# Performance work log

Measured on AMD Instinct MI355X. Metric: run time of the kernel, lower is better.

Reference implementation:

```python
import jax, jax.numpy as jnp
import numpy as np
from jax import lax

KS = 5           # gaussian kernel size
PAD = KS // 2
WINDOW_SIZES = (1, 3, 5)
LN_EPS = 1e-5


def _layernorm(x, g, b):
    m = jnp.mean(x, axis=-1, keepdims=True)
    v = jnp.var(x, axis=-1, keepdims=True)
    return (x - m) * lax.rsqrt(v + LN_EPS) * g + b


def _find_best_interval(p):
    # p: (bs, L). Replicates the sequential strictly-greater update over
    # window sizes [1,3,5] and starts 0..L-w: first candidate (in that order)
    bs, L = p.shape
    amax = jnp.argmax(p, axis=1)                                   # (bs,)
    cs = jnp.concatenate([jnp.zeros((bs, 1), p.dtype), jnp.cumsum(p, axis=1)], axis=1)
    scores, starts, widths = [], [], []
    for w in WINDOW_SIZES:
        if w > L // 2:
            continue
        st = jnp.arange(L - w + 1)
        s = cs[:, st + w] - cs[:, st]                              # sliding sums
        contains = (amax[:, None] >= st[None, :]) & (amax[:, None] < st[None, :] + w)
        scores.append(jnp.where(contains, s, -jnp.inf))
        starts.append(st)
        widths.append(jnp.full((L - w + 1,), w, dtype=jnp.int32))
    S = jnp.concatenate(scores, axis=1)                            # (bs, n_cand)
    starts = jnp.concatenate(starts)
    widths = jnp.concatenate(widths)
    best = jnp.argmax(S, axis=1)
    s0 = starts[best]
    e0 = s0 + widths[best]
    return jnp.stack([s0, e0], axis=1)                             # (bs, 2)


def _forward(v, qa, vp_g, vp_b, vp_W, vp_bias, qp_g, qp_b, qp_W, qp_bias,
             gr_g, gr_b, gr_W1, gr_b1, gr_W2, gr_b2, sigma):
    # v: (bs, L, D), qa: (bs, D). Linears stored as (in, out).
    v2 = jax.nn.gelu(_layernorm(v, vp_g, vp_b) @ vp_W + vp_bias, approximate=False)
    qa2 = jax.nn.gelu(_layernorm(qa, qp_g, qp_b) @ qp_W + qp_bias, approximate=False)
    gate = jnp.tanh(jnp.einsum('bld,bd->bl', v2, qa2))[..., None]  # (bs, L, 1)
    h = _layernorm(v2 * gate, gr_g, gr_b)
    h = jax.nn.gelu(h @ gr_W1 + gr_b1, approximate=False)
    logits = h @ gr_W2 + gr_b2                                     # (bs, L, 1)
    kp = jax.nn.softmax(logits, axis=1)                            # softmax over frames
    # adaptive gaussian smoothing over frames
    x = jnp.arange(KS, dtype=jnp.float32) - KS // 2
    kern = jnp.exp(-0.5 * (x / sigma) ** 2)
    kern = (kern / kern.sum()).reshape(1, 1, KS)
    sm = lax.conv_general_dilated(kp.transpose(0, 2, 1), kern, (1,), [(PAD, PAD)],
                                  dimension_numbers=('NCH', 'OIH', 'NCH')).transpose(0, 2, 1)
    gs = jax.nn.softmax(sm, axis=1)[..., 0]                        # (bs, L)
    max_idx = _find_best_interval(gs)
    bs, L = gs.shape
    rng = jnp.arange(L)[None, :]
    mask = (rng >= max_idx[:, 0:1]) & (rng <= max_idx[:, 1:2])
    start_t = max_idx[:, 0].astype(jnp.float32) / 31.0
    end_t = max_idx[:, 1].astype(jnp.float32) / 31.0
    ori_key = logits[..., 0]
    return gs, max_idx, start_t, end_t, mask, ori_key


def setup_inputs() -> dict:
    key = jax.random.key(0)
    ks = jax.random.split(key, 8)
    BS, L, D = 4096, 32, 768
    H = D // 2
    s = 0.02
    return {
        'v': jax.random.normal(ks[0], (BS, L, D), jnp.float32),
        'qa': jax.random.normal(ks[1], (BS, D), jnp.float32),
        'vp_g': jnp.ones((D,), jnp.float32), 'vp_b': jnp.zeros((D,), jnp.float32),
        'vp_W': jax.random.normal(ks[2], (D, D), jnp.float32) * s,
        'vp_bias': jnp.zeros((D,), jnp.float32),
        'qp_g': jnp.ones((D,), jnp.float32), 'qp_b': jnp.zeros((D,), jnp.float32),
        'qp_W': jax.random.normal(ks[3], (D, D), jnp.float32) * s,
        'qp_bias': jnp.zeros((D,), jnp.float32),
        'gr_g': jnp.ones((D,), jnp.float32), 'gr_b': jnp.zeros((D,), jnp.float32),
        'gr_W1': jax.random.normal(ks[4], (D, H), jnp.float32) * s,
        'gr_b1': jnp.zeros((H,), jnp.float32),
        'gr_W2': jax.random.normal(ks[5], (H, 1), jnp.float32) * s,
        'gr_b2': jnp.zeros((1,), jnp.float32),
        'sigma': jnp.asarray(1.0, jnp.float32),
    }


def reference(v, qa, vp_g, vp_b, vp_W, vp_bias, qp_g, qp_b, qp_W, qp_bias,
              gr_g, gr_b, gr_W1, gr_b1, gr_W2, gr_b2, sigma):
    return _forward(v, qa, vp_g, vp_b, vp_W, vp_bias, qp_g, qp_b, qp_W, qp_bias,
                    gr_g, gr_b, gr_W1, gr_b1, gr_W2, gr_b2, sigma)
```

## Files before the change

kernel.cpp:

```cpp
#include <hip/hip_runtime.h>
#include <math.h>

#define DD 768
#define HH 384
#define LL 32
#define BSZ 4096
#define CAP 256
#define EPS_DEC 4e-7

typedef _Float16 half8 __attribute__((ext_vector_type(8)));
typedef _Float16 half4 __attribute__((ext_vector_type(4)));
typedef float floatx4 __attribute__((ext_vector_type(4)));

static __device__ __forceinline__ float geluf(float x) {
    return 0.5f * x * (1.0f + erff(x * 0.70710678118654752440f));
}
static __device__ __forceinline__ double gelud(double x) {
    return 0.5 * x * (1.0 + erf(x * 0.70710678118654752440));
}

static __device__ void tail_fp64(const double* lgd, double sigma, double* gsd,
                                 int* pst, int* pen, int* pflag, double eps) {
    double kern[5];
    {
        double inv = 1.0 / sigma, ssum = 0.;
#pragma unroll
        for (int j = 0; j < 5; j++) {
            double t = (double)(j - 2) * inv;
            kern[j] = exp(-0.5 * t * t);
            ssum += kern[j];
        }
#pragma unroll
        for (int j = 0; j < 5; j++) kern[j] /= ssum;
    }
    double kp[32];
    {
        double mx = lgd[0];
        for (int i = 1; i < 32; i++) mx = fmax(mx, lgd[i]);
        double sum = 0.;
        for (int i = 0; i < 32; i++) { kp[i] = exp(lgd[i] - mx); sum += kp[i]; }
        for (int i = 0; i < 32; i++) kp[i] /= sum;
    }
    double sm[32];
    for (int i = 0; i < 32; i++) {
        double a = 0.;
#pragma unroll
        for (int j = 0; j < 5; j++) {
            int t = i + j - 2;
            if (t >= 0 && t < 32) a += kern[j] * kp[t];
        }
        sm[i] = a;
    }
    {
        double mx = sm[0];
        for (int i = 1; i < 32; i++) mx = fmax(mx, sm[i]);
        double sum = 0.;
        for (int i = 0; i < 32; i++) { gsd[i] = exp(sm[i] - mx); sum += gsd[i]; }
        for (int i = 0; i < 32; i++) gsd[i] /= sum;
    }
    int am = 0;
    double bv = gsd[0];
    for (int i = 1; i < 32; i++)
        if (gsd[i] > bv) { bv = gsd[i]; am = i; }
    int flag = 0;
    if (eps > 0.) {
        double second = -INFINITY;
        for (int i = 0; i < 32; i++)
            if (i != am && gsd[i] > second) second = gsd[i];
        if (bv - second < eps) flag = 1;
    }
    double cs[33];
    cs[0] = 0.;
    double c = 0.;
    for (int i = 0; i < 32; i++) { c += gsd[i]; cs[i + 1] = c; }
    double best = -INFINITY;
    int bs0 = 0, be0 = 0;
    const int wsz[3] = {1, 3, 5};
    for (int wi = 0; wi < 3; wi++) {
        int w = wsz[wi];
        for (int st = 0; st <= 32 - w; st++) {
            if (am >= st && am < st + w) {
                double sc = cs[st + w] - cs[st];
                if (sc > best) { best = sc; bs0 = st; be0 = st + w; }
            }
        }
    }
    if (eps > 0.) {
        int near = 0;
        for (int wi = 0; wi < 3; wi++) {
            int w = wsz[wi];
            for (int st = 0; st <= 32 - w; st++) {
                if (am >= st && am < st + w) {
                    double sc = cs[st + w] - cs[st];
                    if (sc > best - eps) near++;
                }
            }
        }
        if (near >= 2) flag = 1;
    }
    *pst = bs0;
    *pen = be0;
    *pflag = flag;
}

static __device__ __forceinline__ void write_outputs(float* out, int b,
                                                     const double* gsd,
                                                     const double* lgd,
                                                     int st0, int en0, int l) {
    float* o_gs = out;
    float* o_idx = out + 131072;
    float* o_st = out + 139264;
    float* o_et = out + 143360;
    float* o_mask = out + 147456;
    float* o_ok = out + 278528;
    if (l < 32) {
        o_gs[(b << 5) + l] = (float)gsd[l];
        o_mask[(b << 5) + l] = (l >= st0 && l <= en0) ? 1.f : 0.f;
        o_ok[(b << 5) + l] = (float)lgd[l];
    }
    if (l == 0) {
        o_idx[(b << 1)] = (float)st0;
        o_idx[(b << 1) + 1] = (float)en0;
        o_st[b] = (float)((double)st0 / 31.0);
        o_et[b] = (float)((double)en0 / 31.0);
    }
}

__global__ __launch_bounds__(256) void row_stats_k(const float* __restrict__ X,
                                                   float* __restrict__ mean,
                                                   float* __restrict__ rstd,
                                                   int nrows) {
    int w = (int)((blockIdx.x * blockDim.x + threadIdx.x) >> 6);
    int lane = threadIdx.x & 63;
    if (w >= nrows) return;
    const float* row = X + (size_t)w * DD;
    double s = 0., q = 0.;
#pragma unroll
    for (int i = 0; i < 3; i++) {
        float4 v = *(const float4*)(row + ((lane + (i << 6)) << 2));
        double a = v.x, b = v.y, c = v.z, d = v.w;
        s += a + b + c + d;
        q += a * a + b * b + c * c + d * d;
    }
#pragma unroll
    for (int m = 1; m < 64; m <<= 1) {
        s += __shfl_xor(s, m, 64);
        q += __shfl_xor(q, m, 64);
    }
    if (lane == 0) {
        double mu = s * (1.0 / 768.0);
        double var = q * (1.0 / 768.0) - mu * mu;
        mean[w] = (float)mu;
        rstd[w] = (float)rsqrt(var + 1e-5);
    }
}

__global__ __launch_bounds__(256) void wsplit_k(const float* __restrict__ W,
                                                unsigned short* __restrict__ hiT,
                                                unsigned short* __restrict__ loT,
                                                int N) {
    __shared__ float t[64][65];
    const int tid = threadIdx.x;
    const int n0 = blockIdx.x << 6, k0 = blockIdx.y << 6;
    const int kr = tid >> 4, nc = (tid & 15) << 2;
#pragma unroll
    for (int i = 0; i < 4; i++) {
        float4 v = *(const float4*)&W[(size_t)(k0 + kr + (i << 4)) * N + n0 + nc];
        t[kr + (i << 4)][nc] = v.x;
        t[kr + (i << 4)][nc + 1] = v.y;
        t[kr + (i << 4)][nc + 2] = v.z;
        t[kr + (i << 4)][nc + 3] = v.w;
    }
    __syncthreads();
    const int nr = tid >> 2, kc = (tid & 3) << 4;
    half8 hv0 = {}, hv1 = {}, lv0 = {}, lv1 = {};
#pragma unroll
    for (int j = 0; j < 8; j++) {
        float x = t[kc + j][nr];
        _Float16 h = (_Float16)x;
        hv0[j] = h;
        lv0[j] = (_Float16)(x - (float)h);
    }
#pragma unroll
    for (int j = 0; j < 8; j++) {
        float x = t[kc + 8 + j][nr];
        _Float16 h = (_Float16)x;
        hv1[j] = h;
        lv1[j] = (_Float16)(x - (float)h);
    }
    size_t base = (size_t)(n0 + nr) * DD + k0 + kc;
    *(half8*)&hiT[base] = hv0;
    *(half8*)&hiT[base + 8] = hv1;
    *(half8*)&loT[base] = lv0;
    *(half8*)&loT[base + 8] = lv1;
}

__global__ __launch_bounds__(256) void gemm_ln_gelu_k(
    const float* __restrict__ A, const float* __restrict__ mean,
    const float* __restrict__ rstd, const float* __restrict__ lng,
    const float* __restrict__ lnb, const unsigned short* __restrict__ WhiT,
    const unsigned short* __restrict__ WloT, const float* __restrict__ bias,
    float* __restrict__ Out) {
    __shared__ _Float16 Ah[4][128][8];
    __shared__ _Float16 Al[4][128][8];
    __shared__ _Float16 Bh[4][128][8];
    __shared__ _Float16 Bl[4][128][8];
    const int tid = threadIdx.x;
    const int m0 = blockIdx.x << 7;
    const int n0 = blockIdx.y << 7;
    const int l = tid & 63;
    const int wv = tid >> 6;
    const int wm = (wv >> 1) << 6;
    const int wn = (wv & 1) << 6;
    const int lm = l & 15, lg = l >> 4;
    const int ar = tid >> 3;
    const int k4 = (tid & 7) << 2;
    const int akg = k4 >> 3, aj = k4 & 7;
    const int br = tid >> 1;
    const int bh16 = (tid & 1) << 4;
    const int bkg = bh16 >> 3;

    float mu[4], rs[4];
#pragma unroll
    for (int i = 0; i < 4; i++) {
        mu[i] = mean[m0 + ar + (i << 5)];
        rs[i] = rstd[m0 + ar + (i << 5)];
    }
    floatx4 acc[4][4] = {};
    const float* Ab = A + (size_t)m0 * DD;
    const unsigned short* WhB = WhiT + (size_t)n0 * DD;
    const unsigned short* WlB = WloT + (size_t)n0 * DD;

    for (int kb = 0; kb < DD; kb += 32) {
        __syncthreads();
        {
            float4 g4 = *(const float4*)&lng[kb + k4];
            float4 b4 = *(const float4*)&lnb[kb + k4];
#pragma unroll
            for (int i = 0; i < 4; i++) {
                int m = ar + (i << 5);
                float4 av = *(const float4*)&Ab[(size_t)m * DD + kb + k4];
                float x0 = (av.x - mu[i]) * rs[i] * g4.x + b4.x;
                float x1 = (av.y - mu[i]) * rs[i] * g4.y + b4.y;
                float x2 = (av.z - mu[i]) * rs[i] * g4.z + b4.z;
                float x3 = (av.w - mu[i]) * rs[i] * g4.w + b4.w;
                _Float16 h0 = (_Float16)x0, h1 = (_Float16)x1;
                _Float16 h2 = (_Float16)x2, h3 = (_Float16)x3;
                half4 hv = {h0, h1, h2, h3};
                half4 lv = {(_Float16)(x0 - (float)h0),
                            (_Float16)(x1 - (float)h1),
                            (_Float16)(x2 - (float)h2),
                            (_Float16)(x3 - (float)h3)};
                *(half4*)&Ah[akg][m][aj] = hv;
                *(half4*)&Al[akg][m][aj] = lv;
            }
        }
        {
            const unsigned short* sh = WhB + (size_t)br * DD + kb + bh16;
            const unsigned short* sl = WlB + (size_t)br * DD + kb + bh16;
            half8 w0 = *(const half8*)sh;
            half8 w1 = *(const half8*)(sh + 8);
            half8 u0 = *(const half8*)sl;
            half8 u1 = *(const half8*)(sl + 8);
            *(half8*)&Bh[bkg][br][0] = w0;
            *(half8*)&Bh[bkg + 1][br][0] = w1;
            *(half8*)&Bl[bkg][br][0] = u0;
            *(half8*)&Bl[bkg + 1][br][0] = u1;
        }
        __syncthreads();
        half8 ah[4], al[4];
#pragma unroll
        for (int mi = 0; mi < 4; mi++) {
            ah[mi] = *(const half8*)&Ah[lg][wm + mi * 16 + lm][0];
            al[mi] = *(const half8*)&Al[lg][wm + mi * 16 + lm][0];
        }
#pragma unroll
        for (int ni = 0; ni < 4; ni++) {
            half8 bhv = *(const half8*)&Bh[lg][wn + ni * 16 + lm][0];
            half8 blv = *(const half8*)&Bl[lg][wn + ni * 16 + lm][0];
#pragma unroll
            for (int mi = 0; mi < 4; mi++) {
                acc[mi][ni] = __builtin_amdgcn_mfma_f32_16x16x32_f16(
                    ah[mi], bhv, acc[mi][ni], 0, 0, 0);
                acc[mi][ni] = __builtin_amdgcn_mfma_f32_16x16x32_f16(
                    ah[mi], blv, acc[mi][ni], 0, 0, 0);
                acc[mi][ni] = __builtin_amdgcn_mfma_f32_16x16x32_f16(
                    al[mi], bhv, acc[mi][ni], 0, 0, 0);
            }
        }
    }

#pragma unroll
    for (int ni = 0; ni < 4; ni++) {
        float bz = bias[n0 + wn + ni * 16 + lm];
#pragma unroll
        for (int mi = 0; mi < 4; mi++) {
#pragma unroll
            for (int r = 0; r < 4; r++) {
                float val = acc[mi][ni][r] + bz;
                int row = m0 + wm + mi * 16 + (lg << 2) + r;
                Out[(size_t)row * DD + n0 + wn + ni * 16 + lm] = geluf(val);
            }
        }
    }
}

__global__ __launch_bounds__(256) void gate_stats_k(
    const float* __restrict__ V2, const float* __restrict__ qa2,
    float* __restrict__ s1, float* __restrict__ s2,
    float* __restrict__ logits, const float* __restrict__ b2,
    int rowbase, int nrows) {
    int r = (int)((blockIdx.x * blockDim.x + threadIdx.x) >> 6);
    int lane = threadIdx.x & 63;
    if (r >= nrows) return;
    const float* vr = V2 + (size_t)r * DD;
    const float* qr = qa2 + (size_t)((rowbase + r) >> 5) * DD;
    double dot = 0., s = 0., q = 0.;
#pragma unroll
    for (int i = 0; i < 3; i++) {
        int idx = (lane + (i << 6)) << 2;
        float4 a = *(const float4*)(vr + idx);
        float4 b = *(const float4*)(qr + idx);
        double ax = a.x, ay = a.y, az = a.z, aw = a.w;
        dot += ax * b.x + ay * b.y + az * b.z + aw * b.w;
        s += ax + ay + az + aw;
        q += ax * ax + ay * ay + az * az + aw * aw;
    }
#pragma unroll
    for (int m = 1; m < 64; m <<= 1) {
        dot += __shfl_xor(dot, m, 64);
        s += __shfl_xor(s, m, 64);
        q += __shfl_xor(q, m, 64);
    }
    double gate = tanh(dot);
    double mu = gate * (s * (1.0 / 768.0));
    double var = gate * gate * (q * (1.0 / 768.0)) - mu * mu;
    double rs = rsqrt(var + 1e-5);
    if (lane == 0) {
        s1[r] = (float)(gate * rs);
        s2[r] = (float)(mu * rs);
        logits[rowbase + r] = b2[0];
    }
}

__global__ __launch_bounds__(256) void gemm_h_logits_k(
    const float* __restrict__ V2, const float* __restrict__ s1,
    const float* __restrict__ s2, const float* __restrict__ gg,
    const float* __restrict__ gb, const unsigned short* __restrict__ WhiT,
    const unsigned short* __restrict__ WloT, const float* __restrict__ b1,
    const float* __restrict__ w2, float* __restrict__ logits) {
    __shared__ _Float16 Ah[4][128][8];
    __shared__ _Float16 Al[4][128][8];
    __shared__ _Float16 Bh[4][128][8];
    __shared__ _Float16 Bl[4][128][8];
    __shared__ float red[128][2];
    const int tid = threadIdx.x;
    const int m0 = blockIdx.x << 7;
    const int n0 = blockIdx.y << 7;
    const int l = tid & 63;
    const int wv = tid >> 6;
    const int wm = (wv >> 1) << 6;
    const int wn = (wv & 1) << 6;
    const int lm = l & 15, lg = l >> 4;
    const int ar = tid >> 3;
    const int k4 = (tid & 7) << 2;
    const int akg = k4 >> 3, aj = k4 & 7;
    const int br = tid >> 1;
    const int bh16 = (tid & 1) << 4;
    const int bkg = bh16 >> 3;

    float ss1[4], ss2[4];
#pragma unroll
    for (int i = 0; i < 4; i++) {
        ss1[i] = s1[m0 + ar + (i << 5)];
        ss2[i] = s2[m0 + ar + (i << 5)];
    }
    floatx4 acc[4][4] = {};
    const float* Ab = V2 + (size_t)m0 * DD;
    const unsigned short* WhB = WhiT + (size_t)n0 * DD;
    const unsigned short* WlB = WloT + (size_t)n0 * DD;

    for (int kb = 0; kb < DD; kb += 32) {
        __syncthreads();
        {
            float4 g4 = *(const float4*)&gg[kb + k4];
            float4 b4 = *(const float4*)&gb[kb + k4];
#pragma unroll
            for (int i = 0; i < 4; i++) {
                int m = ar + (i << 5);
                float4 av = *(const float4*)&Ab[(size_t)m * DD + kb + k4];
                float x0 = g4.x * (av.x * ss1[i] - ss2[i]) + b4.x;
                float x1 = g4.y * (av.y * ss1[i] - ss2[i]) + b4.y;
                float x2 = g4.z * (av.z * ss1[i] - ss2[i]) + b4.z;
                float x3 = g4.w * (av.w * ss1[i] - ss2[i]) + b4.w;
                _Float16 h0 = (_Float16)x0, h1 = (_Float16)x1;
                _Float16 h2 = (_Float16)x2, h3 = (_Float16)x3;
                half4 hv = {h0, h1, h2, h3};
                half4 lv = {(_Float16)(x0 - (float)h0),
                            (_Float16)(x1 - (float)h1),
                            (_Float16)(x2 - (float)h2),
                            (_Float16)(x3 - (float)h3)};
                *(half4*)&Ah[akg][m][aj] = hv;
                *(half4*)&Al[akg][m][aj] = lv;
            }
        }
        {
            const unsigned short* sh = WhB + (size_t)br * DD + kb + bh16;
            const unsigned short* sl = WlB + (size_t)br * DD + kb + bh16;
            half8 w0 = *(const half8*)sh;
            half8 w1 = *(const half8*)(sh + 8);
            half8 u0 = *(const half8*)sl;
            half8 u1 = *(const half8*)(sl + 8);
            *(half8*)&Bh[bkg][br][0] = w0;
            *(half8*)&Bh[bkg + 1][br][0] = w1;
            *(half8*)&Bl[bkg][br][0] = u0;
            *(half8*)&Bl[bkg + 1][br][0] = u1;
        }
        __syncthreads();
        half8 ah[4], al[4];
#pragma unroll
        for (int mi = 0; mi < 4; mi++) {
            ah[mi] = *(const half8*)&Ah[lg][wm + mi * 16 + lm][0];
            al[mi] = *(const half8*)&Al[lg][wm + mi * 16 + lm][0];
        }
#pragma unroll
        for (int ni = 0; ni < 4; ni++) {
            half8 bhv = *(const half8*)&Bh[lg][wn + ni * 16 + lm][0];
            half8 blv = *(const half8*)&Bl[lg][wn + ni * 16 + lm][0];
#pragma unroll
            for (int mi = 0; mi < 4; mi++) {
                acc[mi][ni] = __builtin_amdgcn_mfma_f32_16x16x32_f16(
                    ah[mi], bhv, acc[mi][ni], 0, 0, 0);
                acc[mi][ni] = __builtin_amdgcn_mfma_f32_16x16x32_f16(
                    ah[mi], blv, acc[mi][ni], 0, 0, 0);
                acc[mi][ni] = __builtin_amdgcn_mfma_f32_16x16x32_f16(
                    al[mi], bhv, acc[mi][ni], 0, 0, 0);
            }
        }
    }

    float bz[4], wz[4];
#pragma unroll
    for (int ni = 0; ni < 4; ni++) {
        int col = n0 + wn + ni * 16 + lm;
        bz[ni] = b1[col];
        wz[ni] = w2[col];
    }
#pragma unroll
    for (int mi = 0; mi < 4; mi++) {
#pragma unroll
        for (int r = 0; r < 4; r++) {
            float p = 0.f;
#pragma unroll
            for (int ni = 0; ni < 4; ni++) {
                float val = acc[mi][ni][r] + bz[ni];
                p += geluf(val) * wz[ni];
            }
#pragma unroll
            for (int off = 1; off < 16; off <<= 1) p += __shfl_xor(p, off, 64);
            if (lm == 0) red[wm + mi * 16 + (lg << 2) + r][wv & 1] = p;
        }
    }
    __syncthreads();
    if (tid < 128) atomicAdd(&logits[m0 + tid], red[tid][0] + red[tid][1]);
}

__global__ __launch_bounds__(64) void finalize_detect_k(
    const float* __restrict__ logits, const float* __restrict__ sigma,
    float* __restrict__ out, int* __restrict__ cnt, int* __restrict__ list) {
    int b = blockIdx.x;
    int l = threadIdx.x;
    __shared__ double lgd[32], gsd[32];
    __shared__ int sb[2];
    if (l < 32) lgd[l] = (double)logits[(b << 5) + l];
    __syncthreads();
    if (l == 0) {
        int st, en, flag;
        tail_fp64(lgd, (double)sigma[0], gsd, &st, &en, &flag, EPS_DEC);
        sb[0] = st;
        sb[1] = en;
        if (flag) {
            int i = atomicAdd(cnt, 1);
            list[i] = b;
        }
    }
    __syncthreads();
    write_outputs(out, b, gsd, lgd, sb[0], sb[1], l);
}

__global__ __launch_bounds__(256) void repair_qa_k(
    const float* __restrict__ qa, const float* __restrict__ qp_g,
    const float* __restrict__ qp_b, const float* __restrict__ qp_W,
    const float* __restrict__ qp_bias, const int* __restrict__ cnt,
    const int* __restrict__ list, double* __restrict__ qa2d) {
    int n = *cnt; if (n > CAP) n = CAP;
    int i = blockIdx.x;
    if (i >= n) return;
    int b = list[i];
    __shared__ double buf[768];
    __shared__ float Ws[8][768];
    __shared__ double sc[8];
    int tid = threadIdx.x;
    double s = 0., q = 0.;
    for (int j = tid; j < 768; j += 256) {
        double x = (double)qa[(size_t)b * 768 + j];
        buf[j] = x; s += x; q += x * x;
    }
#pragma unroll
    for (int m = 1; m < 64; m <<= 1) {
        s += __shfl_xor(s, m, 64);
        q += __shfl_xor(q, m, 64);
    }
    if ((tid & 63) == 0) { sc[tid >> 6] = s; sc[4 + (tid >> 6)] = q; }
    __syncthreads();
    double S = sc[0] + sc[1] + sc[2] + sc[3];
    double Q = sc[4] + sc[5] + sc[6] + sc[7];
    double mu = S * (1.0 / 768.0);
    double rs = rsqrt(Q * (1.0 / 768.0) - mu * mu + 1e-5);
    for (int j = tid; j < 768; j += 256)
        buf[j] = (buf[j] - mu) * rs * (double)qp_g[j] + (double)qp_b[j];
    __syncthreads();
    {
        double acc0 = 0., acc1 = 0., acc2 = 0.;
        for (int k0 = 0; k0 < 768; k0 += 8) {
            __syncthreads();
            const float4* src = (const float4*)(qp_W + (size_t)k0 * 768);
#pragma unroll
            for (int t = 0; t < 6; t++)
                ((float4*)Ws)[tid + (t << 8)] = src[tid + (t << 8)];
            __syncthreads();
#pragma unroll
            for (int u = 0; u < 8; u++) {
                double a = buf[k0 + u];
                acc0 = fma(a, (double)Ws[u][tid], acc0);
                acc1 = fma(a, (double)Ws[u][tid + 256], acc1);
                acc2 = fma(a, (double)Ws[u][tid + 512], acc2);
            }
        }
        qa2d[(size_t)i * 768 + tid] = gelud(acc0 + (double)qp_bias[tid]);
        qa2d[(size_t)i * 768 + tid + 256] = gelud(acc1 + (double)qp_bias[tid + 256]);
        qa2d[(size_t)i * 768 + tid + 512] = gelud(acc2 + (double)qp_bias[tid + 512]);
    }
}

__global__ __launch_bounds__(256) void repair_v2_k(
    const float* __restrict__ v, const float* __restrict__ vp_g,
    const float* __restrict__ vp_b, const float* __restrict__ vp_W,
    const float* __restrict__ vp_bias, const int* __restrict__ cnt,
    const int* __restrict__ list, double* __restrict__ v2d) {
    int n = *cnt; if (n > CAP) n = CAP;
    int i = blockIdx.x >> 3, rg = blockIdx.x & 7;
    if (i >= n) return;
    int b = list[i];
    __shared__ double A[4][768];
    __shared__ float Ws[8][768];
    __shared__ double sc[8];
    int tid = threadIdx.x;
    for (int r = 0; r < 4; r++) {
        const float* vr = v + ((size_t)(b * 32 + rg * 4 + r)) * 768;
        double s = 0., q = 0.;
        for (int j = tid; j < 768; j += 256) {
            double x = (double)vr[j];
            A[r][j] = x; s += x; q += x * x;
        }
#pragma unroll
        for (int m = 1; m < 64; m <<= 1) {
            s += __shfl_xor(s, m, 64);
            q += __shfl_xor(q, m, 64);
        }
        if ((tid & 63) == 0) { sc[tid >> 6] = s; sc[4 + (tid >> 6)] = q; }
        __syncthreads();
        double S = sc[0] + sc[1] + sc[2] + sc[3];
        double Q = sc[4] + sc[5] + sc[6] + sc[7];
        double mu = S * (1.0 / 768.0);
        double rs = rsqrt(Q * (1.0 / 768.0) - mu * mu + 1e-5);
        for (int j = tid; j < 768; j += 256)
            A[r][j] = (A[r][j] - mu) * rs * (double)vp_g[j] + (double)vp_b[j];
        __syncthreads();
    }
    {
        double acc[3][4] = {};
        for (int k0 = 0; k0 < 768; k0 += 8) {
            __syncthreads();
            const float4* src = (const float4*)(vp_W + (size_t)k0 * 768);
#pragma unroll
            for (int t = 0; t < 6; t++)
                ((float4*)Ws)[tid + (t << 8)] = src[tid + (t << 8)];
            __syncthreads();
#pragma unroll
            for (int u = 0; u < 8; u++) {
                double w0 = (double)Ws[u][tid];
                double w1 = (double)Ws[u][tid + 256];
                double w2_ = (double)Ws[u][tid + 512];
#pragma unroll
                for (int r = 0; r < 4; r++) {
                    double a = A[r][k0 + u];
                    acc[0][r] = fma(a, w0, acc[0][r]);
                    acc[1][r] = fma(a, w1, acc[1][r]);
                    acc[2][r] = fma(a, w2_, acc[2][r]);
                }
            }
        }
        size_t base = (size_t)i * 32 + rg * 4;
#pragma unroll
        for (int jj = 0; jj < 3; jj++) {
            int j = tid + (jj << 8);
            double bias = (double)vp_bias[j];
#pragma unroll
            for (int r = 0; r < 4; r++)
                v2d[(base + r) * 768 + j] = gelud(acc[jj][r] + bias);
        }
    }
}

__global__ __launch_bounds__(256) void repair_h_k(
    const double* __restrict__ v2d, const double* __restrict__ qa2d,
    const float* __restrict__ gr_g, const float* __restrict__ gr_b,
    const float* __restrict__ gr_W1, const float* __restrict__ gr_b1,
    const float* __restrict__ gr_W2, const float* __restrict__ gr_b2,
    const int* __restrict__ cnt, const int* __restrict__ list,
    double* __restrict__ lgd_out) {
    int n = *cnt; if (n > CAP) n = CAP;
    int i = blockIdx.x >> 3, rg = blockIdx.x & 7;
    if (i >= n) return;
    __shared__ double A[4][768];
    __shared__ float Ws[8][512];
    __shared__ double sc[12];
    __shared__ double red[4][4];
    int tid = threadIdx.x;
    const double* qrow = qa2d + (size_t)i * 768;
    for (int r = 0; r < 4; r++) {
        const double* vr = v2d + ((size_t)i * 32 + rg * 4 + r) * 768;
        double s = 0., q = 0., dot = 0.;
        for (int j = tid; j < 768; j += 256) {
            double x = vr[j];
            A[r][j] = x; s += x; q += x * x; dot += x * qrow[j];
        }
#pragma unroll
        for (int m = 1; m < 64; m <<= 1) {
            s += __shfl_xor(s, m, 64);
            q += __shfl_xor(q, m, 64);
            dot += __shfl_xor(dot, m, 64);
        }
        if ((tid & 63) == 0) {
            int w = tid >> 6;
            sc[w] = s; sc[4 + w] = q; sc[8 + w] = dot;
        }
        __syncthreads();
        double S = sc[0] + sc[1] + sc[2] + sc[3];
        double Q = sc[4] + sc[5] + sc[6] + sc[7];
        double Dt = sc[8] + sc[9] + sc[10] + sc[11];
        double gate = tanh(Dt);
        double mu = gate * (S * (1.0 / 768.0));
        double var = gate * gate * (Q * (1.0 / 768.0)) - mu * mu;
        double rs = rsqrt(var + 1e-5);
        double s1v = gate * rs, s2v = mu * rs;
        for (int j = tid; j < 768; j += 256)
            A[r][j] = (double)gr_g[j] * (A[r][j] * s1v - s2v) + (double)gr_b[j];
        __syncthreads();
    }
    double part[4] = {};
    {
        const bool hi = (tid < 128);
        double acc[2][4] = {};
        for (int k0 = 0; k0 < 768; k0 += 8) {
            __syncthreads();
            const float* src = gr_W1 + (size_t)k0 * 384;
#pragma unroll
            for (int t = 0; t < 3; t++) {
                int f = tid + (t << 8);
                int kr = f / 96;
                int fc = (f - kr * 96) << 2;
                *(float4*)&Ws[kr][fc] = *(const float4*)&src[(size_t)kr * 384 + fc];
            }
            __syncthreads();
#pragma unroll
            for (int u = 0; u < 8; u++) {
                double w0 = (double)Ws[u][tid];
                double w1 = hi ? (double)Ws[u][tid + 256] : 0.;
#pragma unroll
                for (int r = 0; r < 4; r++) {
                    double a = A[r][k0 + u];
                    acc[0][r] = fma(a, w0, acc[0][r]);
                    acc[1][r] = fma(a, w1, acc[1][r]);
                }
            }
        }
        {
            double b1 = (double)gr_b1[tid], w2 = (double)gr_W2[tid];
#pragma unroll
            for (int r = 0; r < 4; r++) part[r] += gelud(acc[0][r] + b1) * w2;
        }
        if (hi) {
            double b1 = (double)gr_b1[tid + 256], w2 = (double)gr_W2[tid + 256];
#pragma unroll
            for (int r = 0; r < 4; r++) part[r] += gelud(acc[1][r] + b1) * w2;
        }
    }
#pragma unroll
    for (int r = 0; r < 4; r++)
#pragma unroll
        for (int m = 1; m < 64; m <<= 1) part[r] += __shfl_xor(part[r], m, 64);
    if ((tid & 63) == 0) {
        int w = tid >> 6;
#pragma unroll
        for (int r = 0; r < 4; r++) red[w][r] = part[r];
    }
    __syncthreads();
    if (tid < 4) {
        double t = red[0][tid] + red[1][tid] + red[2][tid] + red[3][tid] +
                   (double)gr_b2[0];
        lgd_out[(size_t)i * 32 + rg * 4 + tid] = t;
    }
}

__global__ __launch_bounds__(64) void repair_fin_k(
    const double* __restrict__ lgd_in, const float* __restrict__ sigma,
    const int* __restrict__ cnt, const int* __restrict__ list,
    float* __restrict__ out) {
    int n = *cnt; if (n > CAP) n = CAP;
    int i = blockIdx.x;
    if (i >= n) return;
    int b = list[i];
    int l = threadIdx.x;
    __shared__ double lgd[32], gsd[32];
    __shared__ int sb[2];
    if (l < 32) lgd[l] = lgd_in[(size_t)i * 32 + l];
    __syncthreads();
    if (l == 0) {
        int st, en, flag;
        tail_fp64(lgd, (double)sigma[0], gsd, &st, &en, &flag, 0.);
        sb[0] = st;
        sb[1] = en;
    }
    __syncthreads();
    write_outputs(out, b, gsd, lgd, sb[0], sb[1], l);
}

__global__ __launch_bounds__(256) void repair_slow_k(
    const float* __restrict__ v, const float* __restrict__ qa,
    const float* __restrict__ vp_g, const float* __restrict__ vp_b,
    const float* __restrict__ vp_W, const float* __restrict__ vp_bias,
    const float* __restrict__ qp_g, const float* __restrict__ qp_b,
    const float* __restrict__ qp_W, const float* __restrict__ qp_bias,
    const float* __restrict__ gr_g, const float* __restrict__ gr_b,
    const float* __restrict__ gr_W1, const float* __restrict__ gr_b1,
    const float* __restrict__ gr_W2, const float* __restrict__ gr_b2,
    const float* __restrict__ sigma, const int* __restrict__ cnt,
    const int* __restrict__ list, float* __restrict__ out) {
    __shared__ double qa2d[768];
    __shared__ double buf[768];
    __shared__ double v2r[768];
    __shared__ double hln[768];
    __shared__ double lgd[32], gsd[32];
    __shared__ double sc[12];
    __shared__ int sb[2];
    const int tid = threadIdx.x;
    const int n = *cnt;

    for (int ii = CAP + blockIdx.x; ii < n; ii += gridDim.x) {
        const int b = list[ii];
        double s = 0., q = 0.;
        for (int j = tid; j < 768; j += 256) {
            double x = (double)qa[(size_t)b * 768 + j];
            buf[j] = x; s += x; q += x * x;
        }
#pragma unroll
        for (int m = 1; m < 64; m <<= 1) {
            s += __shfl_xor(s, m, 64);
            q += __shfl_xor(q, m, 64);
        }
        if ((tid & 63) == 0) { sc[tid >> 6] = s; sc[4 + (tid >> 6)] = q; }
        __syncthreads();
        {
            double S = sc[0] + sc[1] + sc[2] + sc[3];
            double Q = sc[4] + sc[5] + sc[6] + sc[7];
            double mu = S * (1.0 / 768.0);
            double rs = rsqrt(Q * (1.0 / 768.0) - mu * mu + 1e-5);
            for (int j = tid; j < 768; j += 256)
                buf[j] = (buf[j] - mu) * rs * (double)qp_g[j] + (double)qp_b[j];
        }
        __syncthreads();
        for (int j = tid; j < 768; j += 256) {
            double acc = 0.;
#pragma unroll 8
            for (int k = 0; k < 768; k++)
                acc = fma(buf[k], (double)qp_W[(size_t)k * 768 + j], acc);
            qa2d[j] = gelud(acc + (double)qp_bias[j]);
        }
        __syncthreads();

        for (int r = 0; r < 32; r++) {
            const float* vr = v + ((size_t)(b * 32 + r)) * 768;
            s = 0.; q = 0.;
            for (int j = tid; j < 768; j += 256) {
                double x = (double)vr[j];
                buf[j] = x; s += x; q += x * x;
            }
#pragma unroll
            for (int m = 1; m < 64; m <<= 1) {
                s += __shfl_xor(s, m, 64);
                q += __shfl_xor(q, m, 64);
            }
            if ((tid & 63) == 0) { sc[tid >> 6] = s; sc[4 + (tid >> 6)] = q; }
            __syncthreads();
            {
                double S = sc[0] + sc[1] + sc[2] + sc[3];
                double Q = sc[4] + sc[5] + sc[6] + sc[7];
                double mu = S * (1.0 / 768.0);
                double rs = rsqrt(Q * (1.0 / 768.0) - mu * mu + 1e-5);
                for (int j = tid; j < 768; j += 256)
                    buf[j] = (buf[j] - mu) * rs * (double)vp_g[j] + (double)vp_b[j];
            }
            __syncthreads();
            for (int j = tid; j < 768; j += 256) {
                double acc = 0.;
#pragma unroll 8
                for (int k = 0; k < 768; k++)
                    acc = fma(buf[k], (double)vp_W[(size_t)k * 768 + j], acc);
                v2r[j] = gelud(acc + (double)vp_bias[j]);
            }
            __syncthreads();
            double dot = 0.;
            s = 0.; q = 0.;
            for (int j = tid; j < 768; j += 256) {
                double x = v2r[j];
                dot += x * qa2d[j]; s += x; q += x * x;
            }
#pragma unroll
            for (int m = 1; m < 64; m <<= 1) {
                dot += __shfl_xor(dot, m, 64);
                s += __shfl_xor(s, m, 64);
                q += __shfl_xor(q, m, 64);
            }
            if ((tid & 63) == 0) {
                sc[tid >> 6] = s;
                sc[4 + (tid >> 6)] = q;
                sc[8 + (tid >> 6)] = dot;
            }
            __syncthreads();
            {
                double S = sc[0] + sc[1] + sc[2] + sc[3];
                double Q = sc[4] + sc[5] + sc[6] + sc[7];
                double Dt = sc[8] + sc[9] + sc[10] + sc[11];
                double gate = tanh(Dt);
                double mu = gate * (S * (1.0 / 768.0));
                double var = gate * gate * (Q * (1.0 / 768.0)) - mu * mu;
                double rs = rsqrt(var + 1e-5);
                double s1v = gate * rs, s2v = mu * rs;
                for (int j = tid; j < 768; j += 256)
                    hln[j] = (double)gr_g[j] * (v2r[j] * s1v - s2v) + (double)gr_b[j];
            }
            __syncthreads();
            double part = 0.;
            for (int j = tid; j < 384; j += 256) {
                double acc = 0.;
#pragma unroll 8
                for (int k = 0; k < 768; k++)
                    acc = fma(hln[k], (double)gr_W1[(size_t)k * 384 + j], acc);
                part += gelud(acc + (double)gr_b1[j]) * (double)gr_W2[j];
            }
#pragma unroll
            for (int m = 1; m < 64; m <<= 1) part += __shfl_xor(part, m, 64);
            if ((tid & 63) == 0) sc[tid >> 6] = part;
            __syncthreads();
            if (tid == 0) lgd[r] = sc[0] + sc[1] + sc[2] + sc[3] + (double)gr_b2[0];
            __syncthreads();
        }
        if (tid == 0) {
            int st, en, flag;
            tail_fp64(lgd, (double)sigma[0], gsd, &st, &en, &flag, 0.);
            sb[0] = st;
            sb[1] = en;
        }
        __syncthreads();
        write_outputs(out, b, gsd, lgd, sb[0], sb[1], tid);
        __syncthreads();
    }
}

extern "C" void kernel_launch(void* const* d_in, const int* in_sizes, int n_in,
                              void* d_out, int out_size, void* d_ws, size_t ws_size,
                              hipStream_t stream) {
    (void)in_sizes; (void)n_in; (void)out_size;
    const float* v = (const float*)d_in[0];
    const float* qa = (const float*)d_in[1];
    const float* vp_g = (const float*)d_in[2];
    const float* vp_b = (const float*)d_in[3];
    const float* vp_W = (const float*)d_in[4];
    const float* vp_bias = (const float*)d_in[5];
    const float* qp_g = (const float*)d_in[6];
    const float* qp_b = (const float*)d_in[7];
    const float* qp_W = (const float*)d_in[8];
    const float* qp_bias = (const float*)d_in[9];
    const float* gr_g = (const float*)d_in[10];
    const float* gr_b = (const float*)d_in[11];
    const float* gr_W1 = (const float*)d_in[12];
    const float* gr_b1 = (const float*)d_in[13];
    const float* gr_W2 = (const float*)d_in[14];
    const float* gr_b2 = (const float*)d_in[15];
    const float* sigma = (const float*)d_in[16];
    float* out = (float*)d_out;

    int* cnt = (int*)d_ws;
    int* list = cnt + 8;
    hipMemsetAsync(d_ws, 0, 32, stream);
    double* qa2d = (double*)((char*)d_ws + 32768);
    double* v2d = qa2d + (size_t)CAP * 768;
    double* lgdr = v2d + (size_t)CAP * 32 * 768;
    unsigned short* qWhi = (unsigned short*)(lgdr + (size_t)CAP * 32);
    unsigned short* qWlo = qWhi + (size_t)DD * DD;
    unsigned short* vWhi = qWlo + (size_t)DD * DD;
    unsigned short* vWlo = vWhi + (size_t)DD * DD;
    unsigned short* w1hi = vWlo + (size_t)DD * DD;
    unsigned short* w1lo = w1hi + (size_t)DD * HH;
    float* p = (float*)(w1lo + (size_t)DD * HH);

    size_t head_floats = (size_t)((char*)p - (char*)d_ws) / 4;
    float* qa_mean = p; p += BSZ;
    float* qa_rstd = p; p += BSZ;
    float* qa2 = p; p += (size_t)BSZ * DD;
    float* logits = p; p += (size_t)BSZ * LL;

    size_t fixed = head_floats + (size_t)BSZ * 2 + (size_t)BSZ * DD + (size_t)BSZ * LL;
    int bpc = 1024;
    while (bpc > 32) {
        size_t rows = (size_t)bpc * LL;
        size_t need = fixed + rows * 4 + rows * DD;
        if (need * sizeof(float) <= ws_size) break;
        bpc >>= 1;
    }
    size_t rows = (size_t)bpc * LL;
    float* v_mean = p; p += rows;
    float* v_rstd = p; p += rows;
    float* s1 = p; p += rows;
    float* s2 = p; p += rows;
    float* v2 = p; p += rows * DD;

    wsplit_k<<<dim3(12, 12), dim3(256), 0, stream>>>(qp_W, qWhi, qWlo, DD);
    wsplit_k<<<dim3(12, 12), dim3(256), 0, stream>>>(vp_W, vWhi, vWlo, DD);
    wsplit_k<<<dim3(6, 12), dim3(256), 0, stream>>>(gr_W1, w1hi, w1lo, HH);

    row_stats_k<<<dim3((unsigned)((BSZ * 64) / 256)), dim3(256), 0, stream>>>(
        qa, qa_mean, qa_rstd, BSZ);
    gemm_ln_gelu_k<<<dim3(BSZ / 128, DD / 128), dim3(256), 0, stream>>>(
        qa, qa_mean, qa_rstd, qp_g, qp_b, qWhi, qWlo, qp_bias, qa2);

    int nch = BSZ / bpc;
    for (int c = 0; c < nch; c++) {
        int rowbase = c * (int)rows;
        const float* vchunk = v + (size_t)rowbase * DD;
        row_stats_k<<<dim3((unsigned)((rows * 64) / 256)), dim3(256), 0, stream>>>(
            vchunk, v_mean, v_rstd, (int)rows);
        gemm_ln_gelu_k<<<dim3((unsigned)(rows / 128), DD / 128), dim3(256), 0, stream>>>(
            vchunk, v_mean, v_rstd, vp_g, vp_b, vWhi, vWlo, vp_bias, v2);
        gate_stats_k<<<dim3((unsigned)((rows * 64) / 256)), dim3(256), 0, stream>>>(
            v2, qa2, s1, s2, logits, gr_b2, rowbase, (int)rows);
        gemm_h_logits_k<<<dim3((unsigned)(rows / 128), HH / 128), dim3(256), 0, stream>>>(
            v2, s1, s2, gr_g, gr_b, w1hi, w1lo, gr_b1, gr_W2, logits + rowbase);
    }
    finalize_detect_k<<<dim3(BSZ), dim3(64), 0, stream>>>(logits, sigma, out, cnt, list);
    repair_qa_k<<<dim3(CAP), dim3(256), 0, stream>>>(
        qa, qp_g, qp_b, qp_W, qp_bias, cnt, list, qa2d);
    repair_v2_k<<<dim3(CAP * 8), dim3(256), 0, stream>>>(
        v, vp_g, vp_b, vp_W, vp_bias, cnt, list, v2d);
    repair_h_k<<<dim3(CAP * 8), dim3(256), 0, stream>>>(
        v2d, qa2d, gr_g, gr_b, gr_W1, gr_b1, gr_W2, gr_b2, cnt, list, lgdr);
    repair_fin_k<<<dim3(CAP), dim3(64), 0, stream>>>(lgdr, sigma, cnt, list, out);
    repair_slow_k<<<dim3(256), dim3(256), 0, stream>>>(
        v, qa, vp_g, vp_b, vp_W, vp_bias, qp_g, qp_b, qp_W, qp_bias,
        gr_g, gr_b, gr_W1, gr_b1, gr_W2, gr_b2, sigma, cnt, list, out);
}
```

Baseline: 2.346 ms.

## Fuse row statistics and gate computation into the GEMM prologues

Removes the separate row_stats and gate_stats kernels. Each GEMM block now computes its rows' mean/rstd (and, for the h GEMM, the gate dot product and the scaled LN factors) in a prologue that reads full rows and reduces across 8 lanes. The gr_b2 bias moves into finalize, and logits is zeroed with a memset. This cuts kernel launches and intermediate buffers. In exchange, each row is re-read and its fp64 stats recomputed by every N-tile block (6 for vp, 3 for h), and the prologue adds per-thread fp64 work.

```diff
diff --git a/kernel.cpp b/kernel.cpp
--- a/kernel.cpp
+++ b/kernel.cpp
@@ -126,35 +126,6 @@
     }
 }
 
-__global__ __launch_bounds__(256) void row_stats_k(const float* __restrict__ X,
-                                                   float* __restrict__ mean,
-                                                   float* __restrict__ rstd,
-                                                   int nrows) {
-    int w = (int)((blockIdx.x * blockDim.x + threadIdx.x) >> 6);
-    int lane = threadIdx.x & 63;
-    if (w >= nrows) return;
-    const float* row = X + (size_t)w * DD;
-    double s = 0., q = 0.;
-#pragma unroll
-    for (int i = 0; i < 3; i++) {
-        float4 v = *(const float4*)(row + ((lane + (i << 6)) << 2));
-        double a = v.x, b = v.y, c = v.z, d = v.w;
-        s += a + b + c + d;
-        q += a * a + b * b + c * c + d * d;
-    }
-#pragma unroll
-    for (int m = 1; m < 64; m <<= 1) {
-        s += __shfl_xor(s, m, 64);
-        q += __shfl_xor(q, m, 64);
-    }
-    if (lane == 0) {
-        double mu = s * (1.0 / 768.0);
-        double var = q * (1.0 / 768.0) - mu * mu;
-        mean[w] = (float)mu;
-        rstd[w] = (float)rsqrt(var + 1e-5);
-    }
-}
-
 __global__ __launch_bounds__(256) void wsplit_k(const float* __restrict__ W,
                                                 unsigned short* __restrict__ hiT,
                                                 unsigned short* __restrict__ loT,
@@ -196,8 +167,7 @@
 }
 
 __global__ __launch_bounds__(256) void gemm_ln_gelu_k(
-    const float* __restrict__ A, const float* __restrict__ mean,
-    const float* __restrict__ rstd, const float* __restrict__ lng,
+    const float* __restrict__ A, const float* __restrict__ lng,
     const float* __restrict__ lnb, const unsigned short* __restrict__ WhiT,
     const unsigned short* __restrict__ WloT, const float* __restrict__ bias,
     float* __restrict__ Out) {
@@ -220,14 +190,32 @@
     const int bh16 = (tid & 1) << 4;
     const int bkg = bh16 >> 3;
 
+    const float* Ab = A + (size_t)m0 * DD;
+
     float mu[4], rs[4];
 #pragma unroll
     for (int i = 0; i < 4; i++) {
-        mu[i] = mean[m0 + ar + (i << 5)];
-        rs[i] = rstd[m0 + ar + (i << 5)];
-    }
+        const float* row = Ab + (size_t)(ar + (i << 5)) * DD;
+        double s = 0., q = 0.;
+#pragma unroll
+        for (int t = 0; t < 24; t++) {
+            float4 v4 = *(const float4*)(row + k4 + (t << 5));
+            double a = v4.x, b = v4.y, c = v4.z, d = v4.w;
+            s += a + b + c + d;
+            q += a * a + b * b + c * c + d * d;
+        }
+#pragma unroll
+        for (int m = 1; m < 8; m <<= 1) {
+            s += __shfl_xor(s, m, 64);
+            q += __shfl_xor(q, m, 64);
+        }
+        double muD = s * (1.0 / 768.0);
+        double var = q * (1.0 / 768.0) - muD * muD;
+        mu[i] = (float)muD;
+        rs[i] = (float)rsqrt(var + 1e-5);
+    }
+
     floatx4 acc[4][4] = {};
-    const float* Ab = A + (size_t)m0 * DD;
     const unsigned short* WhB = WhiT + (size_t)n0 * DD;
     const unsigned short* WlB = WloT + (size_t)n0 * DD;
 
@@ -305,50 +293,12 @@
     }
 }
 
-__global__ __launch_bounds__(256) void gate_stats_k(
+__global__ __launch_bounds__(256) void gemm_h_logits_k(
     const float* __restrict__ V2, const float* __restrict__ qa2,
-    float* __restrict__ s1, float* __restrict__ s2,
-    float* __restrict__ logits, const float* __restrict__ b2,
-    int rowbase, int nrows) {
-    int r = (int)((blockIdx.x * blockDim.x + threadIdx.x) >> 6);
-    int lane = threadIdx.x & 63;
-    if (r >= nrows) return;
-    const float* vr = V2 + (size_t)r * DD;
-    const float* qr = qa2 + (size_t)((rowbase + r) >> 5) * DD;
-    double dot = 0., s = 0., q = 0.;
-#pragma unroll
-    for (int i = 0; i < 3; i++) {
-        int idx = (lane + (i << 6)) << 2;
-        float4 a = *(const float4*)(vr + idx);
-        float4 b = *(const float4*)(qr + idx);
-        double ax = a.x, ay = a.y, az = a.z, aw = a.w;
-        dot += ax * b.x + ay * b.y + az * b.z + aw * b.w;
-        s += ax + ay + az + aw;
-        q += ax * ax + ay * ay + az * az + aw * aw;
-    }
-#pragma unroll
-    for (int m = 1; m < 64; m <<= 1) {
-        dot += __shfl_xor(dot, m, 64);
-        s += __shfl_xor(s, m, 64);
-        q += __shfl_xor(q, m, 64);
-    }
-    double gate = tanh(dot);
-    double mu = gate * (s * (1.0 / 768.0));
-    double var = gate * gate * (q * (1.0 / 768.0)) - mu * mu;
-    double rs = rsqrt(var + 1e-5);
-    if (lane == 0) {
-        s1[r] = (float)(gate * rs);
-        s2[r] = (float)(mu * rs);
-        logits[rowbase + r] = b2[0];
-    }
-}
-
-__global__ __launch_bounds__(256) void gemm_h_logits_k(
-    const float* __restrict__ V2, const float* __restrict__ s1,
-    const float* __restrict__ s2, const float* __restrict__ gg,
-    const float* __restrict__ gb, const unsigned short* __restrict__ WhiT,
+    const float* __restrict__ gg, const float* __restrict__ gb,
+    const unsigned short* __restrict__ WhiT,
     const unsigned short* __restrict__ WloT, const float* __restrict__ b1,
-    const float* __restrict__ w2, float* __restrict__ logits) {
+    const float* __restrict__ w2, float* __restrict__ logits, int rowbase) {
     __shared__ _Float16 Ah[4][128][8];
     __shared__ _Float16 Al[4][128][8];
     __shared__ _Float16 Bh[4][128][8];
@@ -369,14 +319,39 @@
     const int bh16 = (tid & 1) << 4;
     const int bkg = bh16 >> 3;
 
+    const float* Ab = V2 + (size_t)m0 * DD;
+
     float ss1[4], ss2[4];
 #pragma unroll
     for (int i = 0; i < 4; i++) {
-        ss1[i] = s1[m0 + ar + (i << 5)];
-        ss2[i] = s2[m0 + ar + (i << 5)];
-    }
+        int grow = rowbase + m0 + ar + (i << 5);
+        const float* row = Ab + (size_t)(ar + (i << 5)) * DD;
+        const float* qrow = qa2 + (size_t)(grow >> 5) * DD;
+        double s = 0., q = 0., dot = 0.;
+#pragma unroll
+        for (int t = 0; t < 24; t++) {
+            float4 a4 = *(const float4*)(row + k4 + (t << 5));
+            float4 b4 = *(const float4*)(qrow + k4 + (t << 5));
+            double ax = a4.x, ay = a4.y, az = a4.z, aw = a4.w;
+            dot += ax * b4.x + ay * b4.y + az * b4.z + aw * b4.w;
+            s += ax + ay + az + aw;
+            q += ax * ax + ay * ay + az * az + aw * aw;
+        }
+#pragma unroll
+        for (int m = 1; m < 8; m <<= 1) {
+            dot += __shfl_xor(dot, m, 64);
+            s += __shfl_xor(s, m, 64);
+            q += __shfl_xor(q, m, 64);
+        }
+        double gate = tanh(dot);
+        double muD = gate * (s * (1.0 / 768.0));
+        double var = gate * gate * (q * (1.0 / 768.0)) - muD * muD;
+        double rsD = rsqrt(var + 1e-5);
+        ss1[i] = (float)(gate * rsD);
+        ss2[i] = (float)(muD * rsD);
+    }
+
     floatx4 acc[4][4] = {};
-    const float* Ab = V2 + (size_t)m0 * DD;
     const unsigned short* WhB = WhiT + (size_t)n0 * DD;
     const unsigned short* WlB = WloT + (size_t)n0 * DD;
 
@@ -466,13 +441,14 @@
 }
 
 __global__ __launch_bounds__(64) void finalize_detect_k(
-    const float* __restrict__ logits, const float* __restrict__ sigma,
-    float* __restrict__ out, int* __restrict__ cnt, int* __restrict__ list) {
+    const float* __restrict__ logits, const float* __restrict__ b2,
+    const float* __restrict__ sigma, float* __restrict__ out,
+    int* __restrict__ cnt, int* __restrict__ list) {
     int b = blockIdx.x;
     int l = threadIdx.x;
     __shared__ double lgd[32], gsd[32];
     __shared__ int sb[2];
-    if (l < 32) lgd[l] = (double)logits[(b << 5) + l];
+    if (l < 32) lgd[l] = (double)logits[(b << 5) + l] + (double)b2[0];
     __syncthreads();
     if (l == 0) {
         int st, en, flag;
@@ -917,49 +893,40 @@
     float* p = (float*)(w1lo + (size_t)DD * HH);
 
     size_t head_floats = (size_t)((char*)p - (char*)d_ws) / 4;
-    float* qa_mean = p; p += BSZ;
-    float* qa_rstd = p; p += BSZ;
     float* qa2 = p; p += (size_t)BSZ * DD;
     float* logits = p; p += (size_t)BSZ * LL;
 
-    size_t fixed = head_floats + (size_t)BSZ * 2 + (size_t)BSZ * DD + (size_t)BSZ * LL;
+    size_t fixed = head_floats + (size_t)BSZ * DD + (size_t)BSZ * LL;
     int bpc = 1024;
     while (bpc > 32) {
         size_t rows = (size_t)bpc * LL;
-        size_t need = fixed + rows * 4 + rows * DD;
+        size_t need = fixed + rows * DD;
         if (need * sizeof(float) <= ws_size) break;
         bpc >>= 1;
     }
     size_t rows = (size_t)bpc * LL;
-    float* v_mean = p; p += rows;
-    float* v_rstd = p; p += rows;
-    float* s1 = p; p += rows;
-    float* s2 = p; p += rows;
     float* v2 = p; p += rows * DD;
 
     wsplit_k<<<dim3(12, 12), dim3(256), 0, stream>>>(qp_W, qWhi, qWlo, DD);
     wsplit_k<<<dim3(12, 12), dim3(256), 0, stream>>>(vp_W, vWhi, vWlo, DD);
     wsplit_k<<<dim3(6, 12), dim3(256), 0, stream>>>(gr_W1, w1hi, w1lo, HH);
 
-    row_stats_k<<<dim3((unsigned)((BSZ * 64) / 256)), dim3(256), 0, stream>>>(
-        qa, qa_mean, qa_rstd, BSZ);
+    hipMemsetAsync(logits, 0, (size_t)BSZ * LL * sizeof(float), stream);
+
     gemm_ln_gelu_k<<<dim3(BSZ / 128, DD / 128), dim3(256), 0, stream>>>(
-        qa, qa_mean, qa_rstd, qp_g, qp_b, qWhi, qWlo, qp_bias, qa2);
+        qa, qp_g, qp_b, qWhi, qWlo, qp_bias, qa2);
 
     int nch = BSZ / bpc;
     for (int c = 0; c < nch; c++) {
         int rowbase = c * (int)rows;
         const float* vchunk = v + (size_t)rowbase * DD;
-        row_stats_k<<<dim3((unsigned)((rows * 64) / 256)), dim3(256), 0, stream>>>(
-            vchunk, v_mean, v_rstd, (int)rows);
         gemm_ln_gelu_k<<<dim3((unsigned)(rows / 128), DD / 128), dim3(256), 0, stream>>>(
-            vchunk, v_mean, v_rstd, vp_g, vp_b, vWhi, vWlo, vp_bias, v2);
-        gate_stats_k<<<dim3((unsigned)((rows * 64) / 256)), dim3(256), 0, stream>>>(
-            v2, qa2, s1, s2, logits, gr_b2, rowbase, (int)rows);
+            vchunk, vp_g, vp_b, vWhi, vWlo, vp_bias, v2);
         gemm_h_logits_k<<<dim3((unsigned)(rows / 128), HH / 128), dim3(256), 0, stream>>>(
-            v2, s1, s2, gr_g, gr_b, w1hi, w1lo, gr_b1, gr_W2, logits + rowbase);
-    }
-    finalize_detect_k<<<dim3(BSZ), dim3(64), 0, stream>>>(logits, sigma, out, cnt, list);
+            v2, qa2, gr_g, gr_b, w1hi, w1lo, gr_b1, gr_W2, logits + rowbase, rowbase);
+    }
+    finalize_detect_k<<<dim3(BSZ), dim3(64), 0, stream>>>(
+        logits, gr_b2, sigma, out, cnt, list);
     repair_qa_k<<<dim3(CAP), dim3(256), 0, stream>>>(
         qa, qp_g, qp_b, qp_W, qp_bias, cnt, list, qa2d);
     repair_v2_k<<<dim3(CAP * 8), dim3(256), 0, stream>>>(
```

Measured after the change: 2.721 ms. +16.0%, slower.
